# Kernel optimization log

Measured on AMD Instinct MI355X. Metric: run time of the kernel, lower is better.

## Reference

```python
import jax, jax.numpy as jnp
import numpy as np

HIDDEN = 1024


def setup_inputs() -> dict:
    key = jax.random.key(0)
    kx, kb, kc = jax.random.split(key, 3)
    x = jax.random.normal(kx, (8, 4096, HIDDEN), dtype=jnp.float32)
    logit_a = jnp.zeros((HIDDEN,), dtype=jnp.float32)
    b = jax.random.normal(kb, (HIDDEN,), dtype=jnp.float32) * 0.1
    c = jax.random.normal(kc, (HIDDEN,), dtype=jnp.float32) * 0.1
    d = jnp.zeros((HIDDEN,), dtype=jnp.float32)
    return {"x": x, "logit_a": logit_a, "b": b, "c": c, "d": d}


def reference(x, logit_a, b, c, d):
    # x: (B, T, D); diagonal SSM: s_t = a*s_{t-1} + b*u_t ; y_t = c*s_t + d*u_t
    B, T, D = x.shape
    a = jnp.tanh(logit_a)  # (D,)

    def step(state, u_t):  # state: (B, D), u_t: (B, D)
        state = state * a + u_t * b
        y_t = state * c + u_t * d
        return state, y_t

    xs = jnp.swapaxes(x, 0, 1)  # (T, B, D)
    init = jnp.zeros((B, D), dtype=x.dtype)
    _, ys = jax.lax.scan(step, init, xs)
    return jnp.swapaxes(ys, 0, 1)  # (B, T, D)
```

## Files before the change

kernel.cpp:

```cpp
#include <hip/hip_runtime.h>
#include <math.h>


#define SSM_B 8
#define SSM_T 4096
#define SSM_D 1024
#define SSM_C 256
#define SSM_L 16

typedef float vfloat4 __attribute__((ext_vector_type(4)));

__device__ __forceinline__ float4 f4_fma(float4 a, float4 s, float4 add) {
    return make_float4(fmaf(a.x, s.x, add.x), fmaf(a.y, s.y, add.y),
                       fmaf(a.z, s.z, add.z), fmaf(a.w, s.w, add.w));
}
__device__ __forceinline__ float4 f4_mul(float4 a, float4 b) {
    return make_float4(a.x * b.x, a.y * b.y, a.z * b.z, a.w * b.w);
}
__device__ __forceinline__ void nt_store_f4(float* p, float4 w) {
    vfloat4 v = {w.x, w.y, w.z, w.w};
    __builtin_nontemporal_store(v, (vfloat4*)p);
}
__device__ __forceinline__ float4 nt_load_f4(const float* p) {
    vfloat4 v = __builtin_nontemporal_load((const vfloat4*)p);
    return make_float4(v.x, v.y, v.z, v.w);
}

__global__ __launch_bounds__(256, 4) void ssm_pass1(
        const float* __restrict__ x, const float* __restrict__ logit_a,
        const float* __restrict__ bco, float* __restrict__ chunk_end) {
    const int k  = blockIdx.x;
    const int bb = blockIdx.y;
    const int d4 = threadIdx.x * 4;

    const float* xp = x + ((size_t)bb * SSM_T + (size_t)k * SSM_L) * SSM_D + d4;

    float4 u[SSM_L];
#pragma unroll
    for (int t = 0; t < SSM_L; ++t)
        u[t] = *(const float4*)(xp + (size_t)t * SSM_D);

    float4 la = *(const float4*)(logit_a + d4);
    float4 bv = *(const float4*)(bco + d4);
    float4 a  = make_float4(tanhf(la.x), tanhf(la.y), tanhf(la.z), tanhf(la.w));

    float4 s = make_float4(0.f, 0.f, 0.f, 0.f);
#pragma unroll
    for (int t = 0; t < SSM_L; ++t) s = f4_fma(a, s, f4_mul(bv, u[t]));

    *(float4*)(chunk_end + ((size_t)k * SSM_B + bb) * SSM_D + d4) = s;
}

__global__ __launch_bounds__(128) void ssm_prefix(
        const float* __restrict__ logit_a,
        const float* __restrict__ chunk_end,
        float* __restrict__ chunk_start) {
    const int tid = blockIdx.x * 128 + threadIdx.x;
    const int d   = tid & (SSM_D - 1);

    float a  = tanhf(logit_a[d]);
    float aL = a;
#pragma unroll
    for (int i = 0; i < 4; ++i) aL *= aL;

    float s = 0.f;
    const size_t stride = (size_t)SSM_B * SSM_D;
    size_t idx = (size_t)tid;
    for (int j0 = 0; j0 < SSM_C; j0 += 16) {
        float ce[16];
#pragma unroll
        for (int i = 0; i < 16; ++i) ce[i] = chunk_end[idx + (size_t)i * stride];
#pragma unroll
        for (int i = 0; i < 16; ++i) {
            chunk_start[idx + (size_t)i * stride] = s;
            s = fmaf(aL, s, ce[i]);
        }
        idx += (size_t)16 * stride;
    }
}

__global__ __launch_bounds__(256, 4) void ssm_pass2(
        const float* __restrict__ x, const float* __restrict__ logit_a,
        const float* __restrict__ bco, const float* __restrict__ cco,
        const float* __restrict__ dco, const float* __restrict__ chunk_start,
        float* __restrict__ y) {
    const int k  = blockIdx.x;
    const int bb = blockIdx.y;
    const int d4 = threadIdx.x * 4;

    const size_t base = ((size_t)bb * SSM_T + (size_t)k * SSM_L) * SSM_D + d4;
    const float* xp = x + base;
    float*       yp = y + base;

    float4 u[SSM_L];
#pragma unroll
    for (int t = 0; t < SSM_L; ++t) u[t] = nt_load_f4(xp + (size_t)t * SSM_D);
    float4 s = *(const float4*)(chunk_start + ((size_t)k * SSM_B + bb) * SSM_D + d4);

    float4 la = *(const float4*)(logit_a + d4);
    float4 bv = *(const float4*)(bco + d4);
    float4 cv = *(const float4*)(cco + d4);
    float4 dv = *(const float4*)(dco + d4);
    float4 a  = make_float4(tanhf(la.x), tanhf(la.y), tanhf(la.z), tanhf(la.w));

#pragma unroll
    for (int t = 0; t < SSM_L; ++t) {
        s = f4_fma(a, s, f4_mul(bv, u[t]));
        u[t] = f4_fma(cv, s, f4_mul(dv, u[t]));
    }

#pragma unroll
    for (int t = 0; t < SSM_L; ++t) nt_store_f4(yp + (size_t)t * SSM_D, u[t]);
}

extern "C" void kernel_launch(void* const* d_in, const int* in_sizes, int n_in,
                              void* d_out, int out_size, void* d_ws, size_t ws_size,
                              hipStream_t stream) {
    const float* x   = (const float*)d_in[0];
    const float* la  = (const float*)d_in[1];
    const float* bco = (const float*)d_in[2];
    const float* cco = (const float*)d_in[3];
    const float* dco = (const float*)d_in[4];
    float* y = (float*)d_out;
    float* chunk_end   = (float*)d_ws;
    float* chunk_start = (float*)d_ws + (size_t)SSM_C * SSM_B * SSM_D;

    dim3 grid(SSM_C, SSM_B);
    dim3 block(256);
    ssm_pass1<<<grid, block, 0, stream>>>(x, la, bco, chunk_end);
    ssm_prefix<<<dim3((SSM_B * SSM_D) / 128), dim3(128), 0, stream>>>(la, chunk_end, chunk_start);
    ssm_pass2<<<grid, block, 0, stream>>>(x, la, bco, cco, dco, chunk_start, y);
}
```

Measured before the change: 264.7 us.

## Use fewer, longer scan chunks processed in register groups of sixteen steps

Chunks go from 256 chunks of 16 steps to 32 chunks of 128 steps. Both passes now walk each chunk in groups of 16 timesteps to keep register use bounded. The prefix kernel shrinks to 32 serial steps over a much smaller chunk-boundary buffer, which cuts workspace traffic and its serial latency. The trade-off is that the main passes launch only 256 blocks of 256 threads, so occupancy is far lower. A memory-bound kernel may then struggle to hide HBM latency, since each wave alternates load, compute and store phases with no overlap.

```diff
diff --git a/kernel.cpp b/kernel.cpp
--- a/kernel.cpp
+++ b/kernel.cpp
@@ -5,8 +5,10 @@
 #define SSM_B 8
 #define SSM_T 4096
 #define SSM_D 1024
-#define SSM_C 256
-#define SSM_L 16
+#define SSM_C 32
+#define SSM_L 128
+#define GRP   16
+#define NGRP  (SSM_L / GRP)
 
 typedef float vfloat4 __attribute__((ext_vector_type(4)));
 
@@ -26,60 +28,59 @@
     return make_float4(v.x, v.y, v.z, v.w);
 }
 
-__global__ __launch_bounds__(256, 4) void ssm_pass1(
+__global__ __launch_bounds__(256, 1) void ssm_pass1(
         const float* __restrict__ x, const float* __restrict__ logit_a,
         const float* __restrict__ bco, float* __restrict__ chunk_end) {
     const int k  = blockIdx.x;
     const int bb = blockIdx.y;
     const int d4 = threadIdx.x * 4;
 
-    const float* xp = x + ((size_t)bb * SSM_T + (size_t)k * SSM_L) * SSM_D + d4;
-
-    float4 u[SSM_L];
-#pragma unroll
-    for (int t = 0; t < SSM_L; ++t)
-        u[t] = *(const float4*)(xp + (size_t)t * SSM_D);
-
     float4 la = *(const float4*)(logit_a + d4);
     float4 bv = *(const float4*)(bco + d4);
     float4 a  = make_float4(tanhf(la.x), tanhf(la.y), tanhf(la.z), tanhf(la.w));
 
-    float4 s = make_float4(0.f, 0.f, 0.f, 0.f);
+    const float* xp = x + ((size_t)bb * SSM_T + (size_t)k * SSM_L) * SSM_D + d4;
+
+    float4 e = make_float4(0.f, 0.f, 0.f, 0.f);
 #pragma unroll
-    for (int t = 0; t < SSM_L; ++t) s = f4_fma(a, s, f4_mul(bv, u[t]));
-
-    *(float4*)(chunk_end + ((size_t)k * SSM_B + bb) * SSM_D + d4) = s;
+    for (int g = 0; g < NGRP; ++g) {
+        float4 u[GRP];
+#pragma unroll
+        for (int t = 0; t < GRP; ++t)
+            u[t] = *(const float4*)(xp + (size_t)(g * GRP + t) * SSM_D);
+#pragma unroll
+        for (int t = 0; t < GRP; ++t) e = f4_fma(a, e, f4_mul(bv, u[t]));
+    }
+    *(float4*)(chunk_end + ((size_t)k * SSM_B + bb) * SSM_D + d4) = e;
 }
 
-__global__ __launch_bounds__(128) void ssm_prefix(
+__global__ __launch_bounds__(256) void ssm_prefix(
         const float* __restrict__ logit_a,
         const float* __restrict__ chunk_end,
         float* __restrict__ chunk_start) {
-    const int tid = blockIdx.x * 128 + threadIdx.x;
+    const int tid = blockIdx.x * 256 + threadIdx.x;
     const int d   = tid & (SSM_D - 1);
 
     float a  = tanhf(logit_a[d]);
     float aL = a;
 #pragma unroll
-    for (int i = 0; i < 4; ++i) aL *= aL;
+    for (int i = 0; i < 7; ++i) aL *= aL;
+
+    const size_t stride = (size_t)SSM_B * SSM_D;
+    float ce[SSM_C];
+#pragma unroll
+    for (int j = 0; j < SSM_C; ++j)
+        ce[j] = chunk_end[(size_t)tid + (size_t)j * stride];
 
     float s = 0.f;
-    const size_t stride = (size_t)SSM_B * SSM_D;
-    size_t idx = (size_t)tid;
-    for (int j0 = 0; j0 < SSM_C; j0 += 16) {
-        float ce[16];
 #pragma unroll
-        for (int i = 0; i < 16; ++i) ce[i] = chunk_end[idx + (size_t)i * stride];
-#pragma unroll
-        for (int i = 0; i < 16; ++i) {
-            chunk_start[idx + (size_t)i * stride] = s;
-            s = fmaf(aL, s, ce[i]);
-        }
-        idx += (size_t)16 * stride;
+    for (int j = 0; j < SSM_C; ++j) {
+        chunk_start[(size_t)tid + (size_t)j * stride] = s;
+        s = fmaf(aL, s, ce[j]);
     }
 }
 
-__global__ __launch_bounds__(256, 4) void ssm_pass2(
+__global__ __launch_bounds__(256, 1) void ssm_pass2(
         const float* __restrict__ x, const float* __restrict__ logit_a,
         const float* __restrict__ bco, const float* __restrict__ cco,
         const float* __restrict__ dco, const float* __restrict__ chunk_start,
@@ -88,29 +89,33 @@
     const int bb = blockIdx.y;
     const int d4 = threadIdx.x * 4;
 
-    const size_t base = ((size_t)bb * SSM_T + (size_t)k * SSM_L) * SSM_D + d4;
-    const float* xp = x + base;
-    float*       yp = y + base;
-
-    float4 u[SSM_L];
-#pragma unroll
-    for (int t = 0; t < SSM_L; ++t) u[t] = nt_load_f4(xp + (size_t)t * SSM_D);
-    float4 s = *(const float4*)(chunk_start + ((size_t)k * SSM_B + bb) * SSM_D + d4);
-
     float4 la = *(const float4*)(logit_a + d4);
     float4 bv = *(const float4*)(bco + d4);
     float4 cv = *(const float4*)(cco + d4);
     float4 dv = *(const float4*)(dco + d4);
     float4 a  = make_float4(tanhf(la.x), tanhf(la.y), tanhf(la.z), tanhf(la.w));
 
-#pragma unroll
-    for (int t = 0; t < SSM_L; ++t) {
-        s = f4_fma(a, s, f4_mul(bv, u[t]));
-        u[t] = f4_fma(cv, s, f4_mul(dv, u[t]));
-    }
+    float4 s = *(const float4*)(chunk_start + ((size_t)k * SSM_B + bb) * SSM_D + d4);
+
+    const size_t base = ((size_t)bb * SSM_T + (size_t)k * SSM_L) * SSM_D + d4;
+    const float* xp = x + base;
+    float*       yp = y + base;
 
 #pragma unroll
-    for (int t = 0; t < SSM_L; ++t) nt_store_f4(yp + (size_t)t * SSM_D, u[t]);
+    for (int g = 0; g < NGRP; ++g) {
+        float4 u[GRP];
+#pragma unroll
+        for (int t = 0; t < GRP; ++t)
+            u[t] = nt_load_f4(xp + (size_t)(g * GRP + t) * SSM_D);
+#pragma unroll
+        for (int t = 0; t < GRP; ++t) {
+            s = f4_fma(a, s, f4_mul(bv, u[t]));
+            u[t] = f4_fma(cv, s, f4_mul(dv, u[t]));
+        }
+#pragma unroll
+        for (int t = 0; t < GRP; ++t)
+            nt_store_f4(yp + (size_t)(g * GRP + t) * SSM_D, u[t]);
+    }
 }
 
 extern "C" void kernel_launch(void* const* d_in, const int* in_sizes, int n_in,
@@ -128,6 +133,6 @@
     dim3 grid(SSM_C, SSM_B);
     dim3 block(256);
     ssm_pass1<<<grid, block, 0, stream>>>(x, la, bco, chunk_end);
-    ssm_prefix<<<dim3((SSM_B * SSM_D) / 128), dim3(128), 0, stream>>>(la, chunk_end, chunk_start);
+    ssm_prefix<<<dim3((SSM_B * SSM_D) / 256), block, 0, stream>>>(la, chunk_end, chunk_start);
     ssm_pass2<<<grid, block, 0, stream>>>(x, la, bco, cco, dco, chunk_start, y);
 }
```

New measurement: 259.6 us. Within noise of the previous version (-1.9%).
